# Kernel optimization log

Hardware: AMD Instinct MI355X
Metric: run time of the kernel (lower is better)

The kernel has to match this reference:

```python
import jax, jax.numpy as jnp
import numpy as np

# Dimensions (match init_kwargs / input_specs)
B, S, D = 4, 2048, 1024
H, DK = 16, 64
CL = 64            # chunk_len
C, N, NL = 32, 2, 128  # chunks, neighbors, neighbor_len
EPS = 1e-5
SCALE = 1.0 / np.sqrt(DK)


def setup_inputs() -> dict:
    key = jax.random.key(0)
    ks = jax.random.split(key, 8)
    w_in = 1.0 / np.sqrt(D)   # xavier-like scale for projections
    return {
        "h": jax.random.normal(ks[0], (B, S, D), jnp.float32),
        "e": jax.random.normal(ks[1], (B, C, N, NL, D), jnp.float32),
        "ln_g": jnp.ones((D,), jnp.float32),
        "ln_b": jnp.zeros((D,), jnp.float32),
        "Wq": jax.random.normal(ks[2], (D, H * DK), jnp.float32) * w_in,
        "bq": jnp.zeros((H * DK,), jnp.float32),
        "Wk": jax.random.normal(ks[3], (D, H * DK), jnp.float32) * w_in,
        "bk": jnp.zeros((H * DK,), jnp.float32),
        "Wv": jax.random.normal(ks[4], (D, H * DK), jnp.float32) * w_in,
        "bv": jnp.zeros((H * DK,), jnp.float32),
        "Wo": jax.random.normal(ks[5], (H * DK, D), jnp.float32) * (1.0 / np.sqrt(H * DK)),
        "bo": jnp.zeros((D,), jnp.float32),
    }


def _layernorm(x, g, b):
    mu = jnp.mean(x, axis=-1, keepdims=True)
    var = jnp.mean(jnp.square(x - mu), axis=-1, keepdims=True)
    return (x - mu) * jax.lax.rsqrt(var + EPS) * g + b


def reference(h, e, ln_g, ln_b, Wq, bq, Wk, bk, Wv, bv, Wo, bo):
    residual = h
    # shift queries so each chunk attends to neighbors retrieved for the previous chunk
    hs = _layernorm(h[:, CL - 1:], ln_g, ln_b)          # [B, S-CL+1, D]
    total = C * CL
    pad = max(0, total - hs.shape[1])
    hp = jnp.pad(hs, ((0, 0), (0, pad), (0, 0))) if pad > 0 else hs[:, :total]
    hb = hp.reshape(B, C, CL, D)                         # [B,C,CL,D]

    q = (hb @ Wq + bq).reshape(B, C, CL, H, DK)
    k = (e @ Wk + bk).reshape(B, C, N, NL, H, DK)
    v = (e @ Wv + bv).reshape(B, C, N, NL, H, DK)

    # scores: [B, C, H, CL, N, NL], softmax over merged (N, NL)
    attn = jnp.einsum('bcihd,bcnjhd->bchinj', q, k) * SCALE
    sh = attn.shape
    attn = jax.nn.softmax(attn.reshape(sh[0], sh[1], sh[2], sh[3], -1), axis=-1).reshape(sh)

    o = jnp.einsum('bchinj,bcnjhd->bcihd', attn, v).reshape(B, C * CL, H * DK)
    o = o @ Wo + bo                                      # [B, C*CL, D]
    # shift output back and crop to original length
    o = jnp.pad(o, ((0, 0), (CL - 1, 0), (0, 0)))[:, :S]
    return o + residual
```

## Files before the change

kernel.cpp:

```cpp
#include <hip/hip_runtime.h>


typedef __attribute__((ext_vector_type(8))) short short8;
typedef __attribute__((ext_vector_type(4))) float f32x4;
typedef unsigned short ushort_t;
typedef unsigned long long u64;

__device__ inline ushort_t f2bf(float f) {
  union { float f; unsigned int u; } v; v.f = f;
  unsigned int u = v.u;
  return (ushort_t)((u + 0x7fffu + ((u >> 16) & 1u)) >> 16);
}
__device__ inline float bf2f(ushort_t s) {
  union { unsigned int u; float f; } v; v.u = ((unsigned int)s) << 16;
  return v.f;
}

__device__ inline void gl_lds16(const void* g, void* l) {
  __builtin_amdgcn_global_load_lds(
      (const __attribute__((address_space(1))) unsigned int*)g,
      (__attribute__((address_space(3))) unsigned int*)l, 16, 0, 0);
}

__global__ void prep_kernel(const float* __restrict__ W0, const float* __restrict__ W1,
                            const float* __restrict__ W2, const float* __restrict__ W3,
                            ushort_t* __restrict__ T0, ushort_t* __restrict__ T1,
                            ushort_t* __restrict__ T2, ushort_t* __restrict__ T3,
                            const float* __restrict__ h, const float* __restrict__ lg,
                            const float* __restrict__ lb, ushort_t* __restrict__ hb,
                            const float* __restrict__ e, ushort_t* __restrict__ e_bf) {
  __shared__ float tile[32][33];
  __shared__ float red[8];
  const int blk = blockIdx.x, t = threadIdx.x;

  if (blk < 4096) {
    const int z = blk >> 10, xy = blk & 1023;
    const float* W = (z == 0) ? W0 : (z == 1) ? W1 : (z == 2) ? W2 : W3;
    ushort_t* WT   = (z == 0) ? T0 : (z == 1) ? T1 : (z == 2) ? T2 : T3;
    int k0 = (xy & 31) * 32, n0 = (xy >> 5) * 32;
    int c = t & 31, r = t >> 5;
#pragma unroll
    for (int p = 0; p < 4; p++)
      tile[r + p * 8][c] = W[(size_t)(k0 + r + p * 8) * 1024 + n0 + c];
    __syncthreads();
#pragma unroll
    for (int p = 0; p < 4; p++)
      WT[(size_t)(n0 + r + p * 8) * 1024 + k0 + c] = f2bf(tile[c][r + p * 8]);
    return;
  }
  if (blk < 12288) {
    int row = blk - 4096;
    int b = row >> 11, jj = row & 2047;
    ushort_t* dst = hb + (size_t)row * 1024;
    if (jj >= 1985) {
      ((unsigned int*)dst)[t] = 0u;
      ((unsigned int*)dst)[t + 256] = 0u;
      return;
    }
    const float* src = h + ((size_t)(b << 11) + jj + 63) * 1024;
    f32x4 x = *(const f32x4*)&src[t * 4];
    float s = x[0] + x[1] + x[2] + x[3];
    float sq = x[0]*x[0] + x[1]*x[1] + x[2]*x[2] + x[3]*x[3];
#pragma unroll
    for (int off = 32; off > 0; off >>= 1) {
      s  += __shfl_xor(s, off);
      sq += __shfl_xor(sq, off);
    }
    if ((t & 63) == 0) { red[(t >> 6) * 2] = s; red[(t >> 6) * 2 + 1] = sq; }
    __syncthreads();
    float sum = red[0] + red[2] + red[4] + red[6];
    float sumsq = red[1] + red[3] + red[5] + red[7];
    float mu = sum * (1.f / 1024.f);
    float var = sumsq * (1.f / 1024.f) - mu * mu;
    float rs = rsqrtf(var + 1e-5f);
    f32x4 gg = *(const f32x4*)&lg[t * 4];
    f32x4 bv = *(const f32x4*)&lb[t * 4];
    ushort_t o0 = f2bf((x[0] - mu) * rs * gg[0] + bv[0]);
    ushort_t o1 = f2bf((x[1] - mu) * rs * gg[1] + bv[1]);
    ushort_t o2 = f2bf((x[2] - mu) * rs * gg[2] + bv[2]);
    ushort_t o3 = f2bf((x[3] - mu) * rs * gg[3] + bv[3]);
    u64 pack = (u64)o0 | ((u64)o1 << 16) | ((u64)o2 << 32) | ((u64)o3 << 48);
    *(u64*)&dst[t * 4] = pack;
    return;
  }
  {
    int i = (blk - 12288) * 256 + t;
    const f32x4* sp = (const f32x4*)(e + (size_t)i * 8);
    f32x4 a = sp[0], b = sp[1];
    short8 o;
    o[0] = (short)f2bf(a[0]); o[1] = (short)f2bf(a[1]);
    o[2] = (short)f2bf(a[2]); o[3] = (short)f2bf(a[3]);
    o[4] = (short)f2bf(b[0]); o[5] = (short)f2bf(b[1]);
    o[6] = (short)f2bf(b[2]); o[7] = (short)f2bf(b[3]);
    *(short8*)(e_bf + (size_t)i * 8) = o;
  }
}

template <int EPI>
__launch_bounds__(256, 2)
__global__ void gemm_bt(const ushort_t* __restrict__ A, const ushort_t* __restrict__ BT,
                        const float* __restrict__ bias, ushort_t* __restrict__ Cb,
                        float* __restrict__ Cf, const float* __restrict__ resid) {
  const int bid = blockIdx.x;
  if (EPI == 1 && bid >= 512) {
    int tt = bid - 512;
    int b = tt / 63, r = tt % 63;
    size_t idx = ((size_t)(b * 2048) + r) * 1024 + threadIdx.x * 4;
    *(f32x4*)&Cf[idx] = *(const f32x4*)&resid[idx];
    return;
  }
  __shared__ __attribute__((aligned(16))) ushort_t lds[32768];
  const int cpx = 64;
  const int swz = (bid & 7) * cpx + (bid >> 3);
  const int tm = (swz >> 3) * 128, tn = (swz & 7) * 128;
  const int t = threadIdx.x, lane = t & 63, wv = t >> 6;
  const int wm = (wv >> 1) * 64, wn = (wv & 1) * 64;
  const int row16 = lane & 15, g = lane >> 4;

  const ushort_t* Agp[4];
  const ushort_t* Bgp[4];
  int destC[4];
#pragma unroll
  for (int p = 0; p < 4; p++) {
    int c = t + 256 * p;
    int r = c >> 3, s = c & 7;
    int srck = (s ^ (r & 7)) * 8;
    destC[p] = c * 8;
    Agp[p] = A + (size_t)(tm + r) * 1024 + srck;
    Bgp[p] = BT + (size_t)(tn + r) * 1024 + srck;
  }
#define STGBT(T) { ushort_t* L_ = lds + ((T) & 1) * 16384; const int k0_ = (T) * 64; \
    gl_lds16(Agp[0] + k0_, L_ + destC[0]); gl_lds16(Agp[1] + k0_, L_ + destC[1]); \
    gl_lds16(Agp[2] + k0_, L_ + destC[2]); gl_lds16(Agp[3] + k0_, L_ + destC[3]); \
    gl_lds16(Bgp[0] + k0_, L_ + 8192 + destC[0]); gl_lds16(Bgp[1] + k0_, L_ + 8192 + destC[1]); \
    gl_lds16(Bgp[2] + k0_, L_ + 8192 + destC[2]); gl_lds16(Bgp[3] + k0_, L_ + 8192 + destC[3]); }

  int aoffk[2][4], boffk[2][4];
#pragma unroll
  for (int kk2 = 0; kk2 < 2; kk2++) {
#pragma unroll
    for (int m = 0; m < 4; m++) {
      int ra = wm + m * 16 + row16;
      aoffk[kk2][m] = ra * 64 + (((g + 4 * kk2)) ^ (ra & 7)) * 8;
    }
#pragma unroll
    for (int n = 0; n < 4; n++) {
      int rb = wn + n * 16 + row16;
      boffk[kk2][n] = 8192 + rb * 64 + (((g + 4 * kk2)) ^ (rb & 7)) * 8;
    }
  }

  f32x4 acc[4][4] = {};
  STGBT(0);
  for (int T = 0; T < 16; ++T) {
    asm volatile("s_waitcnt vmcnt(0)" ::: "memory");
    __builtin_amdgcn_s_barrier();
    if (T < 15) STGBT(T + 1);
    const ushort_t* Lb = lds + (T & 1) * 16384;
#pragma unroll
    for (int kk2 = 0; kk2 < 2; kk2++) {
      short8 af[4], bfv[4];
#pragma unroll
      for (int n = 0; n < 4; n++) bfv[n] = *(const short8*)&Lb[boffk[kk2][n]];
#pragma unroll
      for (int m = 0; m < 4; m++) af[m] = *(const short8*)&Lb[aoffk[kk2][m]];
      __builtin_amdgcn_s_setprio(1);
#pragma unroll
      for (int m = 0; m < 4; m++)
#pragma unroll
        for (int n = 0; n < 4; n++)
          acc[m][n] = __builtin_amdgcn_mfma_f32_16x16x32_bf16(af[m], bfv[n], acc[m][n], 0, 0, 0);
      __builtin_amdgcn_s_setprio(0);
    }
  }
#undef STGBT

  const int cr = g * 4, cc = row16;
  if (EPI == 0) {
    const int cb = tn + wn;
    float bsv[4];
#pragma unroll
    for (int n = 0; n < 4; n++) bsv[n] = bias[cb + n * 16 + cc];
#pragma unroll
    for (int m = 0; m < 4; m++) {
      int rbase = tm + wm + m * 16 + cr;
#pragma unroll
      for (int j = 0; j < 4; j++) {
        u64 pack = (u64)f2bf(acc[m][0][j] + bsv[0])
                 | ((u64)f2bf(acc[m][1][j] + bsv[1]) << 16)
                 | ((u64)f2bf(acc[m][2][j] + bsv[2]) << 32)
                 | ((u64)f2bf(acc[m][3][j] + bsv[3]) << 48);
        *(u64*)&Cb[(size_t)(rbase + j) * 1024 + cb + cc * 4] = pack;
      }
    }
  } else {
#pragma unroll
    for (int m = 0; m < 4; m++) {
#pragma unroll
      for (int n = 0; n < 4; n++) {
        int col = tn + wn + n * 16 + cc;
        float bsv = bias[col];
#pragma unroll
        for (int j = 0; j < 4; j++) {
          int rg = tm + wm + m * 16 + cr + j;
          float v = acc[m][n][j] + bsv;
          int b = rg >> 11, jj = rg & 2047;
          if (jj < 1985) {
            size_t oi = ((size_t)(b << 11) + jj + 63) * 1024 + col;
            Cf[oi] = v + resid[oi];
          }
        }
      }
    }
  }
}

__launch_bounds__(512, 2)
__global__ void kv_attn(const ushort_t* __restrict__ A, const ushort_t* __restrict__ WkvT,
                        const float* __restrict__ bk, const float* __restrict__ bv,
                        const ushort_t* __restrict__ Qb, ushort_t* __restrict__ Ob) {
  __shared__ __attribute__((aligned(16))) ushort_t smem[75776];
  ushort_t* lds = smem;
  const int bid = blockIdx.x;
  const int swz = (bid & 7) * 128 + (bid >> 3);
  const int bc = swz >> 3, hp = swz & 7;
  const int tm = bc * 256;
  const int t = threadIdx.x, lane = t & 63, wv = t >> 6;
  const int wm = wv >> 2, wn = wv & 3;
  const int row16 = lane & 15, g = lane >> 4;

  {
    const int hb2q = t >> 8, tlq = t & 255;
    ushort_t* QsH = smem + 67584 + hb2q * 4096;
    size_t qbase = ((size_t)bc * 64) * 1024 + (hp * 2 + hb2q) * 64;
    int ch = tlq, r = ch >> 3, gq = (ch & 7) ^ (r & 7);
    gl_lds16(Qb + qbase + (size_t)r * 1024 + gq * 8, &QsH[ch * 8]);
    ch = tlq + 256; r = ch >> 3; gq = (ch & 7) ^ (r & 7);
    gl_lds16(Qb + qbase + (size_t)r * 1024 + gq * 8, &QsH[ch * 8]);
  }

  const ushort_t* Agp[4];
  const ushort_t* Bgp[4];
  int destC[4];
#pragma unroll
  for (int p = 0; p < 4; p++) {
    int c = t + 512 * p;
    int r = c >> 3, s = c & 7;
    int srck = (s ^ (r & 7)) * 8;
    destC[p] = c * 8;
    Agp[p] = A + (size_t)(tm + r) * 1024 + srck;
    int grow = (r < 128) ? (hp * 128 + r) : (1024 + hp * 128 + (r - 128));
    Bgp[p] = WkvT + (size_t)grow * 1024 + srck;
  }
#define STG64(T) { ushort_t* L_ = lds + ((T) & 1) * 32768; const int k0_ = (T) * 64; \
    gl_lds16(Agp[0] + k0_, L_ + destC[0]); gl_lds16(Agp[1] + k0_, L_ + destC[1]); \
    gl_lds16(Agp[2] + k0_, L_ + destC[2]); gl_lds16(Agp[3] + k0_, L_ + destC[3]); \
    gl_lds16(Bgp[0] + k0_, L_ + 16384 + destC[0]); gl_lds16(Bgp[1] + k0_, L_ + 16384 + destC[1]); \
    gl_lds16(Bgp[2] + k0_, L_ + 16384 + destC[2]); gl_lds16(Bgp[3] + k0_, L_ + 16384 + destC[3]); }

  int aoffk[2][8], boffk[2][4];
#pragma unroll
  for (int kk2 = 0; kk2 < 2; kk2++) {
#pragma unroll
    for (int m = 0; m < 8; m++) {
      int ra = wm * 128 + m * 16 + row16;
      aoffk[kk2][m] = ra * 64 + (((g + 4 * kk2)) ^ (ra & 7)) * 8;
    }
#pragma unroll
    for (int n = 0; n < 4; n++) {
      int rb = wn * 64 + n * 16 + row16;
      boffk[kk2][n] = 16384 + rb * 64 + (((g + 4 * kk2)) ^ (rb & 7)) * 8;
    }
  }

  f32x4 acc[8][4] = {};
  STG64(0);
  for (int T = 0; T < 16; ++T) {
    asm volatile("s_waitcnt vmcnt(0)" ::: "memory");
    __builtin_amdgcn_s_barrier();
    if (T < 15) STG64(T + 1);
    const ushort_t* Lb = lds + (T & 1) * 32768;
#pragma unroll
    for (int kk2 = 0; kk2 < 2; kk2++) {
      short8 af[8], bfv[4];
#pragma unroll
      for (int n = 0; n < 4; n++) bfv[n] = *(const short8*)&Lb[boffk[kk2][n]];
#pragma unroll
      for (int m = 0; m < 8; m++) af[m] = *(const short8*)&Lb[aoffk[kk2][m]];
      __builtin_amdgcn_s_setprio(1);
#pragma unroll
      for (int m = 0; m < 8; m++)
#pragma unroll
        for (int n = 0; n < 4; n++)
          acc[m][n] = __builtin_amdgcn_mfma_f32_16x16x32_bf16(af[m], bfv[n], acc[m][n], 0, 0, 0);
      __builtin_amdgcn_s_setprio(0);
    }
  }
#undef STG64

  __syncthreads();

  if (wn < 2) {
    ushort_t* KsH = smem + wn * 16896;
    float bsv[4];
#pragma unroll
    for (int n = 0; n < 4; n++) bsv[n] = bk[hp * 128 + wn * 64 + n * 16 + row16];
#pragma unroll
    for (int m = 0; m < 8; m++) {
      int krow0 = wm * 128 + m * 16 + g * 4;
#pragma unroll
      for (int j = 0; j < 4; j++) {
        int krow = krow0 + j;
        u64 pack = (u64)f2bf(acc[m][0][j] + bsv[0])
                 | ((u64)f2bf(acc[m][1][j] + bsv[1]) << 16)
                 | ((u64)f2bf(acc[m][2][j] + bsv[2]) << 32)
                 | ((u64)f2bf(acc[m][3][j] + bsv[3]) << 48);
        int sl = ((row16 >> 1) ^ (krow & 7)) * 8 + (row16 & 1) * 4;
        *(u64*)&KsH[krow * 64 + sl] = pack;
      }
    }
  } else {
    ushort_t* VtH = smem + 33792 + (wn & 1) * 16896;
    float bsv[4];
#pragma unroll
    for (int n = 0; n < 4; n++) bsv[n] = bv[hp * 128 + (wn - 2) * 64 + n * 16 + row16];
#pragma unroll
    for (int m = 0; m < 8; m++) {
      int krow0 = wm * 128 + m * 16 + g * 4;
#pragma unroll
      for (int n = 0; n < 4; n++) {
        int od = n * 16 + row16;
        u64 pack = (u64)f2bf(acc[m][n][0] + bsv[n])
                 | ((u64)f2bf(acc[m][n][1] + bsv[n]) << 16)
                 | ((u64)f2bf(acc[m][n][2] + bsv[n]) << 32)
                 | ((u64)f2bf(acc[m][n][3] + bsv[n]) << 48);
        *(u64*)&VtH[od * 264 + krow0] = pack;
      }
    }
  }
  __syncthreads();

  const int tl = t & 255, hb2 = t >> 8;
  const int wvL = tl >> 6, laneL = tl & 63;
  ushort_t* QsH = smem + 67584 + hb2 * 4096;
  ushort_t* KsH = smem + hb2 * 16896;
  ushort_t* SpH = KsH;
  ushort_t* VtH = smem + 33792 + hb2 * 16896;

  const int rowA = laneL & 15, kgA = (laneL >> 4) * 8;
  const int cswz = (rowA & 7) << 3;
  f32x4 accs[4][4] = {};
#pragma unroll
  for (int kk = 0; kk < 64; kk += 32) {
    int cq = ((kk + kgA) ^ cswz);
    short8 af[4], bfr[4];
#pragma unroll
    for (int m = 0; m < 4; m++) af[m] = *(const short8*)&QsH[(m * 16 + rowA) * 64 + cq];
#pragma unroll
    for (int n = 0; n < 4; n++)
      bfr[n] = *(const short8*)&KsH[(wvL * 64 + n * 16 + rowA) * 64 + cq];
#pragma unroll
    for (int m = 0; m < 4; m++)
#pragma unroll
      for (int n = 0; n < 4; n++)
        accs[m][n] = __builtin_amdgcn_mfma_f32_16x16x32_bf16(af[m], bfr[n], accs[m][n], 0, 0, 0);
  }
  __syncthreads();

  {
    const int cr = (laneL >> 4) * 4, cc = laneL & 15;
#pragma unroll
    for (int m = 0; m < 4; m++)
#pragma unroll
      for (int n = 0; n < 4; n++)
#pragma unroll
        for (int j = 0; j < 4; j++)
          SpH[(m * 16 + cr + j) * 264 + wvL * 64 + n * 16 + cc] = f2bf(accs[m][n][j]);
  }
  __syncthreads();

  {
    const int r = tl >> 2, q = tl & 3;
    const int base = r * 264 + q * 64;
    float ev[64];
#pragma unroll
    for (int p = 0; p < 8; p++) {
      short8 sv = *(const short8*)&SpH[base + p * 8];
#pragma unroll
      for (int i = 0; i < 8; i++) ev[p * 8 + i] = bf2f((ushort_t)sv[i]);
    }
    float mx = ev[0];
#pragma unroll
    for (int i = 1; i < 64; i++) mx = fmaxf(mx, ev[i]);
    mx = fmaxf(mx, __shfl_xor(mx, 1));
    mx = fmaxf(mx, __shfl_xor(mx, 2));
    float sum = 0.f;
#pragma unroll
    for (int i = 0; i < 64; i++) {
      ev[i] = __expf((ev[i] - mx) * 0.125f);
      sum += ev[i];
    }
    sum += __shfl_xor(sum, 1);
    sum += __shfl_xor(sum, 2);
    float inv = 1.f / sum;
#pragma unroll
    for (int p = 0; p < 8; p++) {
      short8 pv;
#pragma unroll
      for (int i = 0; i < 8; i++) pv[i] = (short)f2bf(ev[p * 8 + i] * inv);
      *(short8*)&SpH[base + p * 8] = pv;
    }
  }
  __syncthreads();

  {
    f32x4 acco[4] = {};
#pragma unroll
    for (int kt = 0; kt < 8; kt++) {
      short8 bfv = *(const short8*)&VtH[(wvL * 16 + rowA) * 264 + kt * 32 + kgA];
#pragma unroll
      for (int m = 0; m < 4; m++) {
        short8 af = *(const short8*)&SpH[(m * 16 + rowA) * 264 + kt * 32 + kgA];
        acco[m] = __builtin_amdgcn_mfma_f32_16x16x32_bf16(af, bfv, acco[m], 0, 0, 0);
      }
    }
    const int cr = (laneL >> 4) * 4, cc = laneL & 15;
    size_t obase = ((size_t)bc * 64) * 1024 + (hp * 2 + hb2) * 64 + wvL * 16 + cc;
#pragma unroll
    for (int m = 0; m < 4; m++)
#pragma unroll
      for (int j = 0; j < 4; j++)
        Ob[obase + (size_t)(m * 16 + cr + j) * 1024] = f2bf(acco[m][j]);
  }
}

extern "C" void kernel_launch(void* const* d_in, const int* in_sizes, int n_in,
                              void* d_out, int out_size, void* d_ws, size_t ws_size,
                              hipStream_t stream) {
  const float* h    = (const float*)d_in[0];
  const float* e    = (const float*)d_in[1];
  const float* ln_g = (const float*)d_in[2];
  const float* ln_b = (const float*)d_in[3];
  const float* Wq   = (const float*)d_in[4];
  const float* bq   = (const float*)d_in[5];
  const float* Wk   = (const float*)d_in[6];
  const float* bk   = (const float*)d_in[7];
  const float* Wv   = (const float*)d_in[8];
  const float* bv   = (const float*)d_in[9];
  const float* Wo   = (const float*)d_in[10];
  const float* bo   = (const float*)d_in[11];
  float* out = (float*)d_out;

  char* ws = (char*)d_ws;
  const size_t MB = 1024 * 1024;
  ushort_t* WqT  = (ushort_t*)(ws + 0 * MB);
  ushort_t* WkT  = (ushort_t*)(ws + 2 * MB);
  ushort_t* WvT  = (ushort_t*)(ws + 4 * MB);
  ushort_t* WoT  = (ushort_t*)(ws + 6 * MB);
  ushort_t* hb   = (ushort_t*)(ws + 8 * MB);
  ushort_t* e_bf = (ushort_t*)(ws + 24 * MB);
  ushort_t* Qb   = (ushort_t*)(ws + 88 * MB);
  ushort_t* Obuf = (ushort_t*)(ws + 104 * MB);

  prep_kernel<<<28672, 256, 0, stream>>>(Wq, Wk, Wv, Wo, WqT, WkT, WvT, WoT,
                                         h, ln_g, ln_b, hb, e, e_bf);

  gemm_bt<0><<<512, 256, 0, stream>>>(hb, WqT, bq, Qb, nullptr, nullptr);
  kv_attn<<<1024, 512, 0, stream>>>(e_bf, WkT, bk, bv, Qb, Obuf);

  gemm_bt<1><<<764, 256, 0, stream>>>(Obuf, WoT, bo, nullptr, out, h);
}
```

Before: 246.9 us.

## Split kv_attn blocks to one head per 256-thread block with K=32 stages

The fused K/V projection and attention kernel now handles one head per block instead of a head pair. It launches 2048 blocks of 256 threads, halving LDS per block and staging K in 32-wide steps with a new swizzle. The aim is more resident blocks per CU and better latency hiding. In exchange, the neighbor activation tile is loaded twice as often, since each block reuses it for only one head, and the loop needs twice as many barriers.

```diff
diff --git a/kernel.cpp b/kernel.cpp
--- a/kernel.cpp
+++ b/kernel.cpp
@@ -215,96 +215,96 @@
   }
 }
 
-__launch_bounds__(512, 2)
+__launch_bounds__(256, 2)
 __global__ void kv_attn(const ushort_t* __restrict__ A, const ushort_t* __restrict__ WkvT,
                         const float* __restrict__ bk, const float* __restrict__ bv,
                         const ushort_t* __restrict__ Qb, ushort_t* __restrict__ Ob) {
-  __shared__ __attribute__((aligned(16))) ushort_t smem[75776];
+  __shared__ __attribute__((aligned(16))) ushort_t smem[37888];
   ushort_t* lds = smem;
   const int bid = blockIdx.x;
-  const int swz = (bid & 7) * 128 + (bid >> 3);
-  const int bc = swz >> 3, hp = swz & 7;
+  const int swz = (bid & 7) * 256 + (bid >> 3);
+  const int bc = swz >> 4, h = swz & 15;
   const int tm = bc * 256;
   const int t = threadIdx.x, lane = t & 63, wv = t >> 6;
-  const int wm = wv >> 2, wn = wv & 3;
+  const int wm = wv >> 1, wn = wv & 1;
   const int row16 = lane & 15, g = lane >> 4;
 
   {
-    const int hb2q = t >> 8, tlq = t & 255;
-    ushort_t* QsH = smem + 67584 + hb2q * 4096;
-    size_t qbase = ((size_t)bc * 64) * 1024 + (hp * 2 + hb2q) * 64;
-    int ch = tlq, r = ch >> 3, gq = (ch & 7) ^ (r & 7);
+    ushort_t* QsH = smem + 33792;
+    size_t qbase = ((size_t)bc * 64) * 1024 + h * 64;
+    int ch = t, r = ch >> 3, gq = (ch & 7) ^ (r & 7);
     gl_lds16(Qb + qbase + (size_t)r * 1024 + gq * 8, &QsH[ch * 8]);
-    ch = tlq + 256; r = ch >> 3; gq = (ch & 7) ^ (r & 7);
+    ch = t + 256; r = ch >> 3; gq = (ch & 7) ^ (r & 7);
     gl_lds16(Qb + qbase + (size_t)r * 1024 + gq * 8, &QsH[ch * 8]);
   }
 
   const ushort_t* Agp[4];
-  const ushort_t* Bgp[4];
-  int destC[4];
+  int destA[4];
 #pragma unroll
   for (int p = 0; p < 4; p++) {
-    int c = t + 512 * p;
-    int r = c >> 3, s = c & 7;
-    int srck = (s ^ (r & 7)) * 8;
-    destC[p] = c * 8;
+    int c = t + 256 * p;
+    int r = c >> 2, s = c & 3;
+    int srck = (s ^ ((r >> 1) & 3)) * 8;
+    destA[p] = c * 8;
     Agp[p] = A + (size_t)(tm + r) * 1024 + srck;
-    int grow = (r < 128) ? (hp * 128 + r) : (1024 + hp * 128 + (r - 128));
+  }
+  const ushort_t* Bgp[2];
+  int destB[2];
+#pragma unroll
+  for (int p = 0; p < 2; p++) {
+    int c = t + 256 * p;
+    int r = c >> 2, s = c & 3;
+    int srck = (s ^ ((r >> 1) & 3)) * 8;
+    destB[p] = 8192 + c * 8;
+    int grow = (r < 64) ? (h * 64 + r) : (1024 + h * 64 + (r - 64));
     Bgp[p] = WkvT + (size_t)grow * 1024 + srck;
   }
-#define STG64(T) { ushort_t* L_ = lds + ((T) & 1) * 32768; const int k0_ = (T) * 64; \
-    gl_lds16(Agp[0] + k0_, L_ + destC[0]); gl_lds16(Agp[1] + k0_, L_ + destC[1]); \
-    gl_lds16(Agp[2] + k0_, L_ + destC[2]); gl_lds16(Agp[3] + k0_, L_ + destC[3]); \
-    gl_lds16(Bgp[0] + k0_, L_ + 16384 + destC[0]); gl_lds16(Bgp[1] + k0_, L_ + 16384 + destC[1]); \
-    gl_lds16(Bgp[2] + k0_, L_ + 16384 + destC[2]); gl_lds16(Bgp[3] + k0_, L_ + 16384 + destC[3]); }
-
-  int aoffk[2][8], boffk[2][4];
-#pragma unroll
-  for (int kk2 = 0; kk2 < 2; kk2++) {
-#pragma unroll
-    for (int m = 0; m < 8; m++) {
-      int ra = wm * 128 + m * 16 + row16;
-      aoffk[kk2][m] = ra * 64 + (((g + 4 * kk2)) ^ (ra & 7)) * 8;
-    }
-#pragma unroll
-    for (int n = 0; n < 4; n++) {
-      int rb = wn * 64 + n * 16 + row16;
-      boffk[kk2][n] = 16384 + rb * 64 + (((g + 4 * kk2)) ^ (rb & 7)) * 8;
-    }
+#define STG32(T) { ushort_t* L_ = lds + ((T) & 1) * 12288; const int k0_ = (T) * 32; \
+    gl_lds16(Agp[0] + k0_, L_ + destA[0]); gl_lds16(Agp[1] + k0_, L_ + destA[1]); \
+    gl_lds16(Agp[2] + k0_, L_ + destA[2]); gl_lds16(Agp[3] + k0_, L_ + destA[3]); \
+    gl_lds16(Bgp[0] + k0_, L_ + destB[0]); gl_lds16(Bgp[1] + k0_, L_ + destB[1]); }
+
+  int aoff[8], boff[4];
+#pragma unroll
+  for (int m = 0; m < 8; m++) {
+    int ra = wm * 128 + m * 16 + row16;
+    aoff[m] = ra * 32 + (g ^ ((ra >> 1) & 3)) * 8;
+  }
+#pragma unroll
+  for (int n = 0; n < 4; n++) {
+    int rb = wn * 64 + n * 16 + row16;
+    boff[n] = 8192 + rb * 32 + (g ^ ((rb >> 1) & 3)) * 8;
   }
 
   f32x4 acc[8][4] = {};
-  STG64(0);
-  for (int T = 0; T < 16; ++T) {
+  STG32(0);
+  for (int T = 0; T < 32; ++T) {
     asm volatile("s_waitcnt vmcnt(0)" ::: "memory");
     __builtin_amdgcn_s_barrier();
-    if (T < 15) STG64(T + 1);
-    const ushort_t* Lb = lds + (T & 1) * 32768;
-#pragma unroll
-    for (int kk2 = 0; kk2 < 2; kk2++) {
-      short8 af[8], bfv[4];
-#pragma unroll
-      for (int n = 0; n < 4; n++) bfv[n] = *(const short8*)&Lb[boffk[kk2][n]];
-#pragma unroll
-      for (int m = 0; m < 8; m++) af[m] = *(const short8*)&Lb[aoffk[kk2][m]];
-      __builtin_amdgcn_s_setprio(1);
-#pragma unroll
-      for (int m = 0; m < 8; m++)
-#pragma unroll
-        for (int n = 0; n < 4; n++)
-          acc[m][n] = __builtin_amdgcn_mfma_f32_16x16x32_bf16(af[m], bfv[n], acc[m][n], 0, 0, 0);
-      __builtin_amdgcn_s_setprio(0);
-    }
-  }
-#undef STG64
+    if (T < 31) STG32(T + 1);
+    const ushort_t* Lb = lds + (T & 1) * 12288;
+    short8 af[8], bfv[4];
+#pragma unroll
+    for (int n = 0; n < 4; n++) bfv[n] = *(const short8*)&Lb[boff[n]];
+#pragma unroll
+    for (int m = 0; m < 8; m++) af[m] = *(const short8*)&Lb[aoff[m]];
+    __builtin_amdgcn_s_setprio(1);
+#pragma unroll
+    for (int m = 0; m < 8; m++)
+#pragma unroll
+      for (int n = 0; n < 4; n++)
+        acc[m][n] = __builtin_amdgcn_mfma_f32_16x16x32_bf16(af[m], bfv[n], acc[m][n], 0, 0, 0);
+    __builtin_amdgcn_s_setprio(0);
+  }
+#undef STG32
 
   __syncthreads();
 
-  if (wn < 2) {
-    ushort_t* KsH = smem + wn * 16896;
+  if (wn == 0) {
+    ushort_t* KsH = smem;
     float bsv[4];
 #pragma unroll
-    for (int n = 0; n < 4; n++) bsv[n] = bk[hp * 128 + wn * 64 + n * 16 + row16];
+    for (int n = 0; n < 4; n++) bsv[n] = bk[h * 64 + n * 16 + row16];
 #pragma unroll
     for (int m = 0; m < 8; m++) {
       int krow0 = wm * 128 + m * 16 + g * 4;
@@ -320,10 +320,10 @@
       }
     }
   } else {
-    ushort_t* VtH = smem + 33792 + (wn & 1) * 16896;
+    ushort_t* VtH = smem + 16896;
     float bsv[4];
 #pragma unroll
-    for (int n = 0; n < 4; n++) bsv[n] = bv[hp * 128 + (wn - 2) * 64 + n * 16 + row16];
+    for (int n = 0; n < 4; n++) bsv[n] = bv[h * 64 + n * 16 + row16];
 #pragma unroll
     for (int m = 0; m < 8; m++) {
       int krow0 = wm * 128 + m * 16 + g * 4;
@@ -340,12 +340,11 @@
   }
   __syncthreads();
 
-  const int tl = t & 255, hb2 = t >> 8;
-  const int wvL = tl >> 6, laneL = tl & 63;
-  ushort_t* QsH = smem + 67584 + hb2 * 4096;
-  ushort_t* KsH = smem + hb2 * 16896;
+  ushort_t* QsH = smem + 33792;
+  ushort_t* KsH = smem;
   ushort_t* SpH = KsH;
-  ushort_t* VtH = smem + 33792 + hb2 * 16896;
+  ushort_t* VtH = smem + 16896;
+  const int wvL = t >> 6, laneL = t & 63;
 
   const int rowA = laneL & 15, kgA = (laneL >> 4) * 8;
   const int cswz = (rowA & 7) << 3;
@@ -380,7 +379,7 @@
   __syncthreads();
 
   {
-    const int r = tl >> 2, q = tl & 3;
+    const int r = t >> 2, q = t & 3;
     const int base = r * 264 + q * 64;
     float ev[64];
 #pragma unroll
@@ -425,7 +424,7 @@
       }
     }
     const int cr = (laneL >> 4) * 4, cc = laneL & 15;
-    size_t obase = ((size_t)bc * 64) * 1024 + (hp * 2 + hb2) * 64 + wvL * 16 + cc;
+    size_t obase = ((size_t)bc * 64) * 1024 + h * 64 + wvL * 16 + cc;
 #pragma unroll
     for (int m = 0; m < 4; m++)
 #pragma unroll
@@ -466,7 +465,7 @@
                                          h, ln_g, ln_b, hb, e, e_bf);
 
   gemm_bt<0><<<512, 256, 0, stream>>>(hb, WqT, bq, Qb, nullptr, nullptr);
-  kv_attn<<<1024, 512, 0, stream>>>(e_bf, WkT, bk, bv, Qb, Obuf);
+  kv_attn<<<2048, 256, 0, stream>>>(e_bf, WkT, bk, bv, Qb, Obuf);
 
   gemm_bt<1><<<764, 256, 0, stream>>>(Obuf, WoT, bo, nullptr, out, h);
 }
```

Result: slower. 257.3 us (+4.2%).
